# Optimization experiments

Hardware: AMD Instinct MI355X
Metric: run time of the kernel (lower is better)

Reference implementation:

```python
import jax, jax.numpy as jnp
import numpy as np

N = 256      # max_num_nodes (padded nodes per graph)
H = 8        # attention heads
F = 128      # feature_dim
L = 9        # n_layers
INFLA = 6.0  # MCL inflation
EPS = 1e-6


def _layernorm(x, g, b):
    mu = x.mean(-1, keepdims=True)
    var = ((x - mu) ** 2).mean(-1, keepdims=True)
    return (x - mu) / jnp.sqrt(var + 1e-5) * g + b


def _get_mcl(adj):
    # Markov-cluster style power iteration with inflation every 3rd step (num=6)
    m = adj / (adj.sum(-1, keepdims=True) + EPS)
    r = m
    for i in range(6):
        r = m @ r
        if (i + 1) % 3 == 0:
            r = r ** INFLA
        r = r / (r.sum(-1, keepdims=True) + EPS)
    return r


def _forward(input_x, edge_attr, gcn_lin_w, gcn_root_emb, gcn_edge_w,
             gcn_norm_g, gcn_norm_b, ln_in_g, ln_in_b, ln_ffn_g, ln_ffn_b,
             mcl_w, q_w, k_w, v_w, merge_w, merge_b,
             ffn_w1, ffn_b1, ffn_w2, ffn_b2, final_g, final_b,
             edge_index, n_counts, root):
    BN = input_x.shape[0]
    B = BN // N
    dh = F // H
    row, col = edge_index[0], edge_index[1]

    # --- adjacency / padding masks (built once, as in GC_T.forward) ---
    valid = jnp.arange(N)[None, :] < n_counts[:, None]                    # [B,N]
    eb, es, et = row // N, row % N, col % N
    adj = jnp.zeros((B, N, N), bool).at[eb, es, et].set(True)
    adj = adj | (jnp.eye(N, dtype=bool)[None] & valid[:, :, None])        # self loops on valid nodes
    pad = ~(valid[:, :, None] & valid[:, None, :])
    pad_bias = jnp.where(pad, -1024.0, 0.0)[..., None]                    # [B,N,N,1] (broadcast over H)
    mcl = _get_mcl(adj.astype(input_x.dtype))[..., None]                  # [B,N,N,1]

    # --- GCN degree normalization (degree of row index, +1) ---
    deg = jnp.zeros((BN,), input_x.dtype).at[row].add(1.0) + 1.0
    dis = deg ** -0.5
    enorm = (dis[row] * dis[col])[:, None]                                # [E,1]

    out = input_x.reshape(B, N, F)
    for i in range(L):
        # ---- GCNConv: gather-relu-scatter message passing ----
        res = out
        h = out.reshape(BN, F) @ gcn_lin_w[i].T                           # [BN,F]
        ee = edge_attr @ gcn_edge_w[i].T                                  # [E,F]
        msg = enorm * jax.nn.relu(h[row] + ee)                            # x_j = x[row]
        agg = jax.ops.segment_sum(msg, col, num_segments=BN)              # aggregate at target
        g = agg + jax.nn.relu(h + gcn_root_emb[i][root]) / deg[:, None]
        g = jax.nn.relu(_layernorm(g, gcn_norm_g[i], gcn_norm_b[i]))
        out = g.reshape(B, N, F) + res

        # ---- Encoder: biased multi-head attention + FFN ----
        bias4 = (pad_bias + mcl * mcl_w[i][:, 0]).transpose(0, 3, 1, 2)   # [B,H,N,N]
        x = out
        q = (x @ q_w[i].T).reshape(B, N, H, dh).transpose(0, 2, 1, 3) * (dh ** -0.5)
        k = (x @ k_w[i].T).reshape(B, N, H, dh).transpose(0, 2, 1, 3)
        v = (x @ v_w[i].T).reshape(B, N, H, dh).transpose(0, 2, 1, 3)
        att = jax.nn.softmax(jnp.einsum('bhnd,bhmd->bhnm', q, k) + bias4, axis=-1)
        o = jnp.einsum('bhnm,bhmd->bhnd', att, v).transpose(0, 2, 1, 3).reshape(B, N, F)
        o = o @ merge_w[i].T + merge_b[i]
        x = _layernorm(o + x, ln_in_g[i], ln_in_b[i])
        f = jax.nn.gelu(x @ ffn_w1[i].T + ffn_b1[i], approximate=False)
        f = f @ ffn_w2[i].T + ffn_b2[i]
        out = _layernorm(x + f, ln_ffn_g[i], ln_ffn_b[i])

    return _layernorm(out, final_g, final_b)


def setup_inputs() -> dict:
    key = jax.random.key(0)
    ks = jax.random.split(key, 16)
    B, E = 16, 65536
    s = 0.02 * L ** -0.5
    w = lambda k, shape: jax.random.normal(k, shape, jnp.float32) * s
    return {
        'input_x': jax.random.normal(ks[0], (B * N, F), jnp.float32),
        'edge_attr': jax.random.normal(ks[1], (E, 7), jnp.float32),
        'gcn_lin_w': w(ks[2], (L, F, F)),
        'gcn_root_emb': jax.random.normal(ks[3], (L, 2, F), jnp.float32) * 0.02,
        'gcn_edge_w': w(ks[4], (L, F, 7)),
        'gcn_norm_g': jnp.ones((L, F), jnp.float32),
        'gcn_norm_b': jnp.zeros((L, F), jnp.float32),
        'ln_in_g': jnp.ones((L, F), jnp.float32),
        'ln_in_b': jnp.zeros((L, F), jnp.float32),
        'ln_ffn_g': jnp.ones((L, F), jnp.float32),
        'ln_ffn_b': jnp.zeros((L, F), jnp.float32),
        'mcl_w': w(ks[5], (L, H, 1)),
        'q_w': w(ks[6], (L, F, F)),
        'k_w': w(ks[7], (L, F, F)),
        'v_w': w(ks[8], (L, F, F)),
        'merge_w': w(ks[9], (L, F, F)),
        'merge_b': jnp.zeros((L, F), jnp.float32),
        'ffn_w1': w(ks[10], (L, 2 * F, F)),
        'ffn_b1': jnp.zeros((L, 2 * F), jnp.float32),
        'ffn_w2': w(ks[11], (L, F, 2 * F)),
        'ffn_b2': jnp.zeros((L, F), jnp.float32),
        'final_g': jnp.ones((F,), jnp.float32),
        'final_b': jnp.zeros((F,), jnp.float32),
        'edge_index': jax.random.randint(ks[12], (2, E), 0, B * N),
        'n_counts': jax.random.randint(ks[13], (B,), 1, N + 1),
        'root': jax.random.randint(ks[14], (B * N,), 0, 2),
    }


def reference(input_x, edge_attr, gcn_lin_w, gcn_root_emb, gcn_edge_w,
              gcn_norm_g, gcn_norm_b, ln_in_g, ln_in_b, ln_ffn_g, ln_ffn_b,
              mcl_w, q_w, k_w, v_w, merge_w, merge_b,
              ffn_w1, ffn_b1, ffn_w2, ffn_b2, final_g, final_b,
              edge_index, n_counts, root):
    return _forward(input_x, edge_attr, gcn_lin_w, gcn_root_emb, gcn_edge_w,
                    gcn_norm_g, gcn_norm_b, ln_in_g, ln_in_b, ln_ffn_g, ln_ffn_b,
                    mcl_w, q_w, k_w, v_w, merge_w, merge_b,
                    ffn_w1, ffn_b1, ffn_w2, ffn_b2, final_g, final_b,
                    edge_index, n_counts, root)
```

## Files before the change

### kernel.cpp

```cpp
#include <hip/hip_runtime.h>
#include <hip/hip_bf16.h>
#include <math.h>

#define NLAYER 9

typedef unsigned short u16;
typedef __attribute__((ext_vector_type(8))) short short8;
typedef __attribute__((ext_vector_type(4))) float f32x4;

__device__ inline u16 f2bf(float x) {
  unsigned int u = __float_as_uint(x);
  unsigned int r = (u + 0x7fffu + ((u >> 16) & 1u)) >> 16;
  return (u16)r;
}
__device__ inline float gelu_exact(float x) {
  return 0.5f * x * (1.0f + erff(x * 0.7071067811865476f));
}

__global__ void build_adj_kernel(const int* __restrict__ ei, float* __restrict__ adj,
                                 float* __restrict__ deg, int* __restrict__ ccount, int E) {
  int e = blockIdx.x * 256 + threadIdx.x;
  if (e >= E) return;
  int r = ei[e], c = ei[E + e];
  int b = r >> 8;
  adj[((size_t)b << 16) + ((size_t)(r & 255) << 8) + (c & 255)] = 1.0f;
  atomicAdd(&deg[r], 1.0f);
  atomicAdd(&ccount[c], 1);
}

__global__ void selfloop_deg_kernel(const int* __restrict__ nc, float* __restrict__ adj,
                                    float* __restrict__ deg, float* __restrict__ dis) {
  int n = blockIdx.x * 256 + threadIdx.x;
  int b = n >> 8, i = n & 255;
  if (i < nc[b]) adj[((size_t)b << 16) + ((size_t)i << 8) + i] = 1.0f;
  float d = deg[n] + 1.0f;
  deg[n] = d;
  dis[n] = rsqrtf(d);
}

__global__ __launch_bounds__(1024) void scan_kernel(const int* __restrict__ ccount,
                                                    int* __restrict__ rowptr, int n) {
  __shared__ int part[1024];
  int t = threadIdx.x;
  int base = t * 4;
  int c[4], s = 0;
#pragma unroll
  for (int i = 0; i < 4; i++) { c[i] = (base + i < n) ? ccount[base + i] : 0; s += c[i]; }
  part[t] = s;
  __syncthreads();
  for (int o = 1; o < 1024; o <<= 1) {
    int v = (t >= o) ? part[t - o] : 0;
    __syncthreads();
    part[t] += v;
    __syncthreads();
  }
  int excl = part[t] - s;
#pragma unroll
  for (int i = 0; i < 4; i++) {
    if (base + i < n) rowptr[base + i] = excl;
    excl += c[i];
  }
  if (t == 1023) rowptr[n] = part[1023];
}

__global__ void scatter_kernel(const int* __restrict__ ei, const float* __restrict__ dis,
                               const int* __restrict__ rowptr, int* __restrict__ fill,
                               int* __restrict__ src_s, int* __restrict__ eidx_s,
                               float* __restrict__ enorm_s, int E) {
  int e = blockIdx.x * 256 + threadIdx.x;
  if (e >= E) return;
  int r = ei[e], c = ei[E + e];
  int pos = rowptr[c] + atomicAdd(&fill[c], 1);
  src_s[pos] = r;
  eidx_s[pos] = e;
  enorm_s[pos] = dis[r] * dis[c];
}

__global__ __launch_bounds__(256) void norm_rows_kernel(const float* __restrict__ src,
                                                        float* __restrict__ dst) {
  int row = blockIdx.x;
  int t = threadIdx.x;
  float v = src[(size_t)row * 256 + t];
  float s = v;
#pragma unroll
  for (int o = 32; o > 0; o >>= 1) s += __shfl_xor(s, o, 64);
  __shared__ float ws4[4];
  if ((t & 63) == 0) ws4[t >> 6] = s;
  __syncthreads();
  float tot = ws4[0] + ws4[1] + ws4[2] + ws4[3];
  dst[(size_t)row * 256 + t] = v / (tot + 1e-6f);
}

__global__ __launch_bounds__(256) void mcl_prep_kernel(const float* __restrict__ m,
                                                       u16* __restrict__ mb,
                                                       u16* __restrict__ rT) {
  int b = blockIdx.z;
  const float* M = m + ((size_t)b << 16);
  u16* MB = mb + ((size_t)b << 16);
  u16* RT = rT + ((size_t)b << 16);
  int r0 = blockIdx.x * 64, c0 = blockIdx.y * 64;
  __shared__ float ts[64][65];
  int t = threadIdx.x;
  int i = t >> 2, jb = (t & 3) * 16;
#pragma unroll
  for (int g = 0; g < 4; g++) {
    int j = jb + g * 4;
    float4 v = *(const float4*)(M + (size_t)(r0 + i) * 256 + c0 + j);
    ts[i][j] = v.x; ts[i][j + 1] = v.y; ts[i][j + 2] = v.z; ts[i][j + 3] = v.w;
    u16 p4[4] = {f2bf(v.x), f2bf(v.y), f2bf(v.z), f2bf(v.w)};
    *(ushort4*)(MB + (size_t)(r0 + i) * 256 + c0 + j) = *(ushort4*)p4;
  }
  __syncthreads();
#pragma unroll
  for (int g = 0; g < 4; g++) {
    int j = jb + g * 4;
    u16 p4[4] = {f2bf(ts[j][i]), f2bf(ts[j + 1][i]), f2bf(ts[j + 2][i]), f2bf(ts[j + 3][i])};
    *(ushort4*)(RT + (size_t)(c0 + i) * 256 + r0 + j) = *(ushort4*)p4;
  }
}

__global__ __launch_bounds__(256) void mcl_iter_kernel(const u16* __restrict__ rT,
                                                       const u16* __restrict__ mb,
                                                       u16* __restrict__ rTn,
                                                       float* __restrict__ mclr,
                                                       int inflate, int fin) {
  __shared__ float red[64];
  int b = blockIdx.x >> 4, i0 = (blockIdx.x & 15) * 16;
  int w = threadIdx.x >> 6, lane = threadIdx.x & 63;
  int m16 = lane & 15, quad = lane >> 4;
  const u16* A = rT + ((size_t)b << 16);
  const u16* Bm = mb + ((size_t)b << 16);
  f32x4 acc[4];
#pragma unroll
  for (int tj = 0; tj < 4; tj++) acc[tj] = (f32x4){0.f, 0.f, 0.f, 0.f};
  for (int k0 = 0; k0 < 256; k0 += 32) {
    short8 bb = *(const short8*)(Bm + (size_t)(i0 + m16) * 256 + k0 + quad * 8);
#pragma unroll
    for (int tj = 0; tj < 4; tj++) {
      short8 a = *(const short8*)(A + (size_t)(w * 64 + tj * 16 + m16) * 256 + k0 + quad * 8);
      acc[tj] = __builtin_amdgcn_mfma_f32_16x16x32_bf16(a, bb, acc[tj], 0, 0, 0);
    }
  }
  float ps = 0.f;
#pragma unroll
  for (int tj = 0; tj < 4; tj++)
#pragma unroll
    for (int reg = 0; reg < 4; reg++) {
      float v = acc[tj][reg];
      if (inflate) { float v2 = v * v; v = v2 * v2 * v2; }
      acc[tj][reg] = v;
      ps += v;
    }
  ps += __shfl_xor(ps, 16, 64);
  ps += __shfl_xor(ps, 32, 64);
  if (quad == 0) red[w * 16 + m16] = ps;
  __syncthreads();
  float tot = red[m16] + red[16 + m16] + red[32 + m16] + red[48 + m16];
  float inv = 1.f / (tot + 1e-6f);
  if (fin) {
    float* dst = mclr + ((size_t)b << 16);
#pragma unroll
    for (int tj = 0; tj < 4; tj++)
#pragma unroll
      for (int reg = 0; reg < 4; reg++) {
        int j = w * 64 + tj * 16 + quad * 4 + reg;
        dst[(size_t)(i0 + m16) * 256 + j] = acc[tj][reg] * inv;
      }
  } else {
    u16* dst = rTn + ((size_t)b << 16);
#pragma unroll
    for (int tj = 0; tj < 4; tj++)
#pragma unroll
      for (int reg = 0; reg < 4; reg++) {
        int j = w * 64 + tj * 16 + quad * 4 + reg;
        dst[(size_t)j * 256 + i0 + m16] = f2bf(acc[tj][reg] * inv);
      }
  }
}

__global__ void conv_w_kernel(const float* __restrict__ s0, const float* __restrict__ s1,
                              const float* __restrict__ s2, const float* __restrict__ s3,
                              const float* __restrict__ s4, const float* __restrict__ s5,
                              const float* __restrict__ s6, u16* __restrict__ d0,
                              u16* __restrict__ d1, u16* __restrict__ d2,
                              u16* __restrict__ d3, u16* __restrict__ d4,
                              u16* __restrict__ d5, u16* __restrict__ d6) {
  int f = blockIdx.y;
  const float* s;
  u16* d;
  int n;
  switch (f) {
    case 0: s = s0; d = d0; n = NLAYER * 4096; break;
    case 1: s = s1; d = d1; n = NLAYER * 4096; break;
    case 2: s = s2; d = d2; n = NLAYER * 4096; break;
    case 3: s = s3; d = d3; n = NLAYER * 4096; break;
    case 4: s = s4; d = d4; n = NLAYER * 4096; break;
    case 5: s = s5; d = d5; n = NLAYER * 8192; break;
    default: s = s6; d = d6; n = NLAYER * 8192; break;
  }
  int stride = gridDim.x * 256;
  for (int i = blockIdx.x * 256 + threadIdx.x; i < n; i += stride) {
    float4 v = ((const float4*)s)[i];
    u16 p4[4] = {f2bf(v.x), f2bf(v.y), f2bf(v.z), f2bf(v.w)};
    ((ushort4*)d)[i] = *(ushort4*)p4;
  }
}

__global__ __launch_bounds__(256) void copyx_lin_kernel(const float* __restrict__ x,
                                                        const u16* __restrict__ wlin0,
                                                        float* __restrict__ outb,
                                                        float* __restrict__ hbuf) {
  __shared__ u16 st[16 * 136];
  int m0 = blockIdx.x * 16;
  int tid = threadIdx.x;
  int w = tid >> 6, lane = tid & 63;
  int m16 = lane & 15, quad = lane >> 4;
  for (int i = tid; i < 2048; i += 256) {
    int row = i >> 7, col = i & 127;
    float v = x[(size_t)(m0 + row) * 128 + col];
    outb[(size_t)(m0 + row) * 128 + col] = v;
    st[row * 136 + col] = f2bf(v);
  }
  __syncthreads();
  int c0 = w * 32;
  f32x4 acc[2] = {{0.f, 0.f, 0.f, 0.f}, {0.f, 0.f, 0.f, 0.f}};
#pragma unroll
  for (int k0 = 0; k0 < 128; k0 += 32) {
    short8 a = *(const short8*)(st + m16 * 136 + k0 + quad * 8);
#pragma unroll
    for (int t = 0; t < 2; t++) {
      short8 bb = *(const short8*)(wlin0 + (size_t)(c0 + t * 16 + m16) * 128 + k0 + quad * 8);
      acc[t] = __builtin_amdgcn_mfma_f32_16x16x32_bf16(a, bb, acc[t], 0, 0, 0);
    }
  }
#pragma unroll
  for (int t = 0; t < 2; t++)
#pragma unroll
    for (int reg = 0; reg < 4; reg++)
      hbuf[(size_t)(m0 + quad * 4 + reg) * 128 + c0 + t * 16 + m16] = acc[t][reg];
}

__global__ __launch_bounds__(256) void gcn_ln_kernel(
    const int* __restrict__ rowptr, const int* __restrict__ src_s,
    const int* __restrict__ eidx_s, const float* __restrict__ enorm_s,
    const float* __restrict__ ea, const float* __restrict__ We, const float* __restrict__ h,
    const float* __restrict__ remb, const int* __restrict__ root,
    const float* __restrict__ deg, const float* __restrict__ gamma,
    const float* __restrict__ beta, float* __restrict__ out, u16* __restrict__ out16) {
  __shared__ float Wt[7 * 128];
  for (int idx = threadIdx.x; idx < 896; idx += 256) {
    int f = idx & 127, k = idx >> 7;
    Wt[k * 128 + f] = We[f * 7 + k];
  }
  __syncthreads();
  int n = blockIdx.x * 4 + (threadIdx.x >> 6);
  int lane = threadIdx.x & 63;
  int f0 = lane, f1 = lane + 64;
  int p0 = rowptr[n], p1 = rowptr[n + 1];
  float a0 = 0.f, a1 = 0.f;
  int r = 0, e = 0;
  float en = 0.f;
  if (p0 < p1) { r = src_s[p0]; e = eidx_s[p0]; en = enorm_s[p0]; }
  for (int p = p0; p < p1; p++) {
    int rn = 0, enx = 0;
    float ennx = 0.f;
    if (p + 1 < p1) { rn = src_s[p + 1]; enx = eidx_s[p + 1]; ennx = enorm_s[p + 1]; }
    const float* eae = ea + (size_t)e * 7;
    float h0 = h[(size_t)r * 128 + f0];
    float h1 = h[(size_t)r * 128 + f1];
    float d0 = 0.f, d1 = 0.f;
#pragma unroll
    for (int k = 0; k < 7; k++) {
      float ev = eae[k];
      d0 += ev * Wt[k * 128 + f0];
      d1 += ev * Wt[k * 128 + f1];
    }
    a0 += en * fmaxf(h0 + d0, 0.f);
    a1 += en * fmaxf(h1 + d1, 0.f);
    r = rn; e = enx; en = ennx;
  }
  float invd = 1.0f / deg[n];
  const float* re = remb + root[n] * 128;
  size_t base = (size_t)n * 128;
  float g0 = a0 + fmaxf(h[base + f0] + re[f0], 0.f) * invd;
  float g1 = a1 + fmaxf(h[base + f1] + re[f1], 0.f) * invd;
  float s = g0 + g1, ss = g0 * g0 + g1 * g1;
#pragma unroll
  for (int o = 32; o > 0; o >>= 1) { s += __shfl_xor(s, o, 64); ss += __shfl_xor(ss, o, 64); }
  float mu = s * 0.0078125f;
  float var = ss * 0.0078125f - mu * mu;
  float rs = rsqrtf(var + 1e-5f);
  float y0 = fmaxf((g0 - mu) * rs * gamma[f0] + beta[f0], 0.f) + out[base + f0];
  float y1 = fmaxf((g1 - mu) * rs * gamma[f1] + beta[f1], 0.f) + out[base + f1];
  out[base + f0] = y0;
  out[base + f1] = y1;
  out16[base + f0] = f2bf(y0);
  out16[base + f1] = f2bf(y1);
}

__global__ __launch_bounds__(256) void mfma_qkv_kernel(const u16* __restrict__ A,
                                                       const u16* __restrict__ qw,
                                                       const u16* __restrict__ kw,
                                                       const u16* __restrict__ vw,
                                                       float* __restrict__ qkv, int BN) {
  int y = blockIdx.y;
  int which = y >> 2;
  const u16* W = (which == 0) ? qw : (which == 1) ? kw : vw;
  float scale = (which == 0) ? 0.25f : 1.0f;
  float* C = qkv + (size_t)which * BN * 128;
  int m0 = blockIdx.x * 64, o0 = (y & 3) * 32;
  int w = threadIdx.x >> 6, lane = threadIdx.x & 63;
  int m16 = lane & 15, quad = lane >> 4;
  const u16* arow = A + (size_t)(m0 + w * 16 + m16) * 128 + quad * 8;
  const u16* brow0 = W + (size_t)(o0 + m16) * 128 + quad * 8;
  const u16* brow1 = W + (size_t)(o0 + 16 + m16) * 128 + quad * 8;
  f32x4 acc0 = {0.f, 0.f, 0.f, 0.f}, acc1 = {0.f, 0.f, 0.f, 0.f};
#pragma unroll
  for (int k0 = 0; k0 < 128; k0 += 32) {
    short8 a = *(const short8*)(arow + k0);
    acc0 = __builtin_amdgcn_mfma_f32_16x16x32_bf16(a, *(const short8*)(brow0 + k0), acc0, 0, 0, 0);
    acc1 = __builtin_amdgcn_mfma_f32_16x16x32_bf16(a, *(const short8*)(brow1 + k0), acc1, 0, 0, 0);
  }
#pragma unroll
  for (int reg = 0; reg < 4; reg++) {
    int row = m0 + w * 16 + quad * 4 + reg;
    C[(size_t)row * 128 + o0 + m16] = acc0[reg] * scale;
    C[(size_t)row * 128 + o0 + 16 + m16] = acc1[reg] * scale;
  }
}

__global__ __launch_bounds__(256) void attn4_kernel(const float* __restrict__ q,
                                                    const float* __restrict__ k,
                                                    const float* __restrict__ v,
                                                    const float* __restrict__ mclr,
                                                    const float* __restrict__ mclw,
                                                    const int* __restrict__ ncnt,
                                                    u16* __restrict__ o) {
  int qt = blockIdx.x, hh = blockIdx.y, b = blockIdx.z;
  int t = threadIdx.x;
  __shared__ float ks[256][16];
  __shared__ float vs[256][16];
  {
    const float* kp = k + ((size_t)(b * 256 + t) * 128 + hh * 16);
    const float* vp = v + ((size_t)(b * 256 + t) * 128 + hh * 16);
#pragma unroll
    for (int d4 = 0; d4 < 16; d4 += 4) {
      *(float4*)&ks[t][d4] = *(const float4*)(kp + d4);
      *(float4*)&vs[t][d4] = *(const float4*)(vp + d4);
    }
  }
  __syncthreads();
  int i = qt * 64 + (t >> 2);
  int d0 = (t & 3) * 4;
  int nc = ncnt[b];
  bool vi = i < nc;
  float wh = mclw[hh];
  const float* qp = q + ((size_t)(b * 256 + i) * 128 + hh * 16 + d0);
  float qv[4] = {qp[0], qp[1], qp[2], qp[3]};
  const float* mrow = mclr + ((size_t)(b * 256 + i)) * 256;
  float acc[4] = {0.f, 0.f, 0.f, 0.f};
  float lsum = 0.f;
  for (int j0 = 0; j0 < 256; j0 += 4) {
    float4 mc = *(const float4*)(mrow + j0);
    float mcv[4] = {mc.x, mc.y, mc.z, mc.w};
#pragma unroll
    for (int jj = 0; jj < 4; jj++) {
      int j = j0 + jj;
      float s = qv[0] * ks[j][d0] + qv[1] * ks[j][d0 + 1] + qv[2] * ks[j][d0 + 2] +
                qv[3] * ks[j][d0 + 3];
      s += __shfl_xor(s, 1, 64);
      s += __shfl_xor(s, 2, 64);
      float bias = mcv[jj] * wh + ((vi && j >= nc) ? -1024.f : 0.f);
      float pe = __expf(s + bias);
      lsum += pe;
      acc[0] += pe * vs[j][d0];
      acc[1] += pe * vs[j][d0 + 1];
      acc[2] += pe * vs[j][d0 + 2];
      acc[3] += pe * vs[j][d0 + 3];
    }
  }
  float inv = 1.f / lsum;
  u16 p4[4] = {f2bf(acc[0] * inv), f2bf(acc[1] * inv), f2bf(acc[2] * inv), f2bf(acc[3] * inv)};
  *(ushort4*)(o + ((size_t)(b * 256 + i) * 128 + hh * 16 + d0)) = *(ushort4*)p4;
}

__global__ __launch_bounds__(256) void merge_ffn1_kernel(
    const u16* __restrict__ ob16, const u16* __restrict__ Wm, const float* __restrict__ mb,
    const float* __restrict__ outb, const float* __restrict__ gam,
    const float* __restrict__ bet, float* __restrict__ xbuf, const u16* __restrict__ W1,
    const float* __restrict__ b1, u16* __restrict__ f116) {
  __shared__ float redS[64], redSS[64];
  __shared__ u16 st[16 * 136];
  int tid = threadIdx.x;
  int w = tid >> 6, lane = tid & 63;
  int m16 = lane & 15, quad = lane >> 4;
  int m0 = blockIdx.x * 16;
  const u16* arow = ob16 + (size_t)(m0 + m16) * 128 + quad * 8;
  f32x4 acc[2] = {{0.f, 0.f, 0.f, 0.f}, {0.f, 0.f, 0.f, 0.f}};
#pragma unroll
  for (int k0 = 0; k0 < 128; k0 += 32) {
    short8 a = *(const short8*)(arow + k0);
#pragma unroll
    for (int t = 0; t < 2; t++) {
      short8 bb = *(const short8*)(Wm + (size_t)(w * 32 + t * 16 + m16) * 128 + k0 + quad * 8);
      acc[t] = __builtin_amdgcn_mfma_f32_16x16x32_bf16(a, bb, acc[t], 0, 0, 0);
    }
  }
  float s4[4] = {0.f, 0.f, 0.f, 0.f}, ss4[4] = {0.f, 0.f, 0.f, 0.f};
#pragma unroll
  for (int t = 0; t < 2; t++) {
    int col = w * 32 + t * 16 + m16;
    float bi = mb[col];
#pragma unroll
    for (int reg = 0; reg < 4; reg++) {
      int row = m0 + quad * 4 + reg;
      float v = acc[t][reg] + bi + outb[(size_t)row * 128 + col];
      acc[t][reg] = v;
      s4[reg] += v;
      ss4[reg] += v * v;
    }
  }
#pragma unroll
  for (int o = 1; o <= 8; o <<= 1)
#pragma unroll
    for (int reg = 0; reg < 4; reg++) {
      s4[reg] += __shfl_xor(s4[reg], o, 64);
      ss4[reg] += __shfl_xor(ss4[reg], o, 64);
    }
  if (m16 == 0) {
#pragma unroll
    for (int reg = 0; reg < 4; reg++) {
      redS[w * 16 + quad * 4 + reg] = s4[reg];
      redSS[w * 16 + quad * 4 + reg] = ss4[reg];
    }
  }
  __syncthreads();
  float mu[4], rsd[4];
#pragma unroll
  for (int reg = 0; reg < 4; reg++) {
    int r = quad * 4 + reg;
    float S = redS[r] + redS[16 + r] + redS[32 + r] + redS[48 + r];
    float SS = redSS[r] + redSS[16 + r] + redSS[32 + r] + redSS[48 + r];
    mu[reg] = S * 0.0078125f;
    float var = SS * 0.0078125f - mu[reg] * mu[reg];
    rsd[reg] = rsqrtf(var + 1e-5f);
  }
#pragma unroll
  for (int t = 0; t < 2; t++) {
    int col = w * 32 + t * 16 + m16;
    float g = gam[col], be = bet[col];
#pragma unroll
    for (int reg = 0; reg < 4; reg++) {
      int row = m0 + quad * 4 + reg;
      float y = (acc[t][reg] - mu[reg]) * rsd[reg] * g + be;
      xbuf[(size_t)row * 128 + col] = y;
      st[(quad * 4 + reg) * 136 + col] = f2bf(y);
    }
  }
  __syncthreads();
  f32x4 acc1[4];
#pragma unroll
  for (int t = 0; t < 4; t++) acc1[t] = (f32x4){0.f, 0.f, 0.f, 0.f};
#pragma unroll
  for (int k0 = 0; k0 < 128; k0 += 32) {
    short8 a = *(const short8*)(st + m16 * 136 + k0 + quad * 8);
#pragma unroll
    for (int t = 0; t < 4; t++) {
      short8 bb = *(const short8*)(W1 + (size_t)(w * 64 + t * 16 + m16) * 128 + k0 + quad * 8);
      acc1[t] = __builtin_amdgcn_mfma_f32_16x16x32_bf16(a, bb, acc1[t], 0, 0, 0);
    }
  }
#pragma unroll
  for (int t = 0; t < 4; t++) {
    int col = w * 64 + t * 16 + m16;
    float bi = b1[col];
#pragma unroll
    for (int reg = 0; reg < 4; reg++) {
      int row = m0 + quad * 4 + reg;
      f116[(size_t)row * 256 + col] = f2bf(gelu_exact(acc1[t][reg] + bi));
    }
  }
}

__global__ __launch_bounds__(256) void ffn2_lin_kernel(
    const u16* __restrict__ f116, const u16* __restrict__ W2, const float* __restrict__ b2,
    const float* __restrict__ xbuf, const float* __restrict__ gam,
    const float* __restrict__ bet, float* __restrict__ outb, const u16* __restrict__ wlin_next,
    float* __restrict__ hbuf) {
  __shared__ float redS[64], redSS[64];
  __shared__ u16 st[16 * 136];
  int tid = threadIdx.x;
  int w = tid >> 6, lane = tid & 63;
  int m16 = lane & 15, quad = lane >> 4;
  int m0 = blockIdx.x * 16;
  const u16* arow = f116 + (size_t)(m0 + m16) * 256 + quad * 8;
  f32x4 acc[2] = {{0.f, 0.f, 0.f, 0.f}, {0.f, 0.f, 0.f, 0.f}};
#pragma unroll
  for (int k0 = 0; k0 < 256; k0 += 32) {
    short8 a = *(const short8*)(arow + k0);
#pragma unroll
    for (int t = 0; t < 2; t++) {
      short8 bb = *(const short8*)(W2 + (size_t)(w * 32 + t * 16 + m16) * 256 + k0 + quad * 8);
      acc[t] = __builtin_amdgcn_mfma_f32_16x16x32_bf16(a, bb, acc[t], 0, 0, 0);
    }
  }
  float s4[4] = {0.f, 0.f, 0.f, 0.f}, ss4[4] = {0.f, 0.f, 0.f, 0.f};
#pragma unroll
  for (int t = 0; t < 2; t++) {
    int col = w * 32 + t * 16 + m16;
    float bi = b2[col];
#pragma unroll
    for (int reg = 0; reg < 4; reg++) {
      int row = m0 + quad * 4 + reg;
      float v = acc[t][reg] + bi + xbuf[(size_t)row * 128 + col];
      acc[t][reg] = v;
      s4[reg] += v;
      ss4[reg] += v * v;
    }
  }
#pragma unroll
  for (int o = 1; o <= 8; o <<= 1)
#pragma unroll
    for (int reg = 0; reg < 4; reg++) {
      s4[reg] += __shfl_xor(s4[reg], o, 64);
      ss4[reg] += __shfl_xor(ss4[reg], o, 64);
    }
  if (m16 == 0) {
#pragma unroll
    for (int reg = 0; reg < 4; reg++) {
      redS[w * 16 + quad * 4 + reg] = s4[reg];
      redSS[w * 16 + quad * 4 + reg] = ss4[reg];
    }
  }
  __syncthreads();
  float mu[4], rsd[4];
#pragma unroll
  for (int reg = 0; reg < 4; reg++) {
    int r = quad * 4 + reg;
    float S = redS[r] + redS[16 + r] + redS[32 + r] + redS[48 + r];
    float SS = redSS[r] + redSS[16 + r] + redSS[32 + r] + redSS[48 + r];
    mu[reg] = S * 0.0078125f;
    float var = SS * 0.0078125f - mu[reg] * mu[reg];
    rsd[reg] = rsqrtf(var + 1e-5f);
  }
#pragma unroll
  for (int t = 0; t < 2; t++) {
    int col = w * 32 + t * 16 + m16;
    float g = gam[col], be = bet[col];
#pragma unroll
    for (int reg = 0; reg < 4; reg++) {
      int row = m0 + quad * 4 + reg;
      float y = (acc[t][reg] - mu[reg]) * rsd[reg] * g + be;
      outb[(size_t)row * 128 + col] = y;
      st[(quad * 4 + reg) * 136 + col] = f2bf(y);
    }
  }
  __syncthreads();
  if (wlin_next) {
    f32x4 acc2[2] = {{0.f, 0.f, 0.f, 0.f}, {0.f, 0.f, 0.f, 0.f}};
#pragma unroll
    for (int k0 = 0; k0 < 128; k0 += 32) {
      short8 a = *(const short8*)(st + m16 * 136 + k0 + quad * 8);
#pragma unroll
      for (int t = 0; t < 2; t++) {
        short8 bb =
            *(const short8*)(wlin_next + (size_t)(w * 32 + t * 16 + m16) * 128 + k0 + quad * 8);
        acc2[t] = __builtin_amdgcn_mfma_f32_16x16x32_bf16(a, bb, acc2[t], 0, 0, 0);
      }
    }
#pragma unroll
    for (int t = 0; t < 2; t++)
#pragma unroll
      for (int reg = 0; reg < 4; reg++)
        hbuf[(size_t)(m0 + quad * 4 + reg) * 128 + w * 32 + t * 16 + m16] = acc2[t][reg];
  }
}

__global__ __launch_bounds__(256) void ln_kernel(const float* __restrict__ a,
                                                 const float* __restrict__ gamma,
                                                 const float* __restrict__ beta,
                                                 float* __restrict__ dst) {
  int n = blockIdx.x * 4 + (threadIdx.x >> 6);
  int lane = threadIdx.x & 63;
  size_t base = (size_t)n * 128;
  int f0 = lane, f1 = lane + 64;
  float x0 = a[base + f0], x1 = a[base + f1];
  float s = x0 + x1, ss = x0 * x0 + x1 * x1;
#pragma unroll
  for (int o = 32; o > 0; o >>= 1) {
    s += __shfl_xor(s, o, 64);
    ss += __shfl_xor(ss, o, 64);
  }
  float mu = s * 0.0078125f;
  float var = ss * 0.0078125f - mu * mu;
  float rs = rsqrtf(var + 1e-5f);
  dst[base + f0] = (x0 - mu) * rs * gamma[f0] + beta[f0];
  dst[base + f1] = (x1 - mu) * rs * gamma[f1] + beta[f1];
}

extern "C" void kernel_launch(void* const* d_in, const int* in_sizes, int n_in,
                              void* d_out, int out_size, void* d_ws, size_t ws_size,
                              hipStream_t stream) {
  const float* input_x = (const float*)d_in[0];
  const float* edge_attr = (const float*)d_in[1];
  const float* gcn_lin_w = (const float*)d_in[2];
  const float* gcn_root = (const float*)d_in[3];
  const float* gcn_edge_w = (const float*)d_in[4];
  const float* gcn_ng = (const float*)d_in[5];
  const float* gcn_nb = (const float*)d_in[6];
  const float* ln_in_g = (const float*)d_in[7];
  const float* ln_in_b = (const float*)d_in[8];
  const float* ln_ffn_g = (const float*)d_in[9];
  const float* ln_ffn_b = (const float*)d_in[10];
  const float* mcl_w = (const float*)d_in[11];
  const float* q_w = (const float*)d_in[12];
  const float* k_w = (const float*)d_in[13];
  const float* v_w = (const float*)d_in[14];
  const float* merge_w = (const float*)d_in[15];
  const float* merge_b = (const float*)d_in[16];
  const float* ffn_w1 = (const float*)d_in[17];
  const float* ffn_b1 = (const float*)d_in[18];
  const float* ffn_w2 = (const float*)d_in[19];
  const float* ffn_b2 = (const float*)d_in[20];
  const float* final_g = (const float*)d_in[21];
  const float* final_b = (const float*)d_in[22];
  const int* edge_index = (const int*)d_in[23];
  const int* n_counts = (const int*)d_in[24];
  const int* root = (const int*)d_in[25];

  const int E = in_sizes[23] / 2;
  const int B = in_sizes[24];
  const int BN = B * 256;

  float* ws = (float*)d_ws;
  size_t off = 0;
  auto alloc = [&](size_t n) {
    off = (off + 3) & ~(size_t)3;
    float* q = ws + off;
    off += n;
    return q;
  };
  const size_t NN2 = (size_t)B * 256 * 256;
  const size_t XF = (size_t)BN * 128;
  float* mclr = alloc(NN2);
  float* mbuf = alloc(NN2);
  float* rt = alloc(NN2);
  (void)rt;
  float* qkv = mbuf;
  float* hbuf = alloc(XF);
  float* xbuf = alloc(XF);
  float* deg = alloc(BN);
  int* ccount = (int*)alloc(BN);
  int* fill = (int*)alloc(BN);
  float* dis = alloc(BN);
  int* rowptr = (int*)alloc(BN + 1);
  int* src_s = (int*)alloc(E);
  int* eidx_s = (int*)alloc(E);
  float* enorm_s = alloc(E);
  u16* mb16 = (u16*)alloc(NN2 / 2);
  u16* rT16 = (u16*)alloc(NN2 / 2);
  u16* cT16 = (u16*)alloc(NN2 / 2);
  u16* outb16 = (u16*)alloc(XF / 2);
  u16* ob16 = (u16*)alloc(XF / 2);
  u16* f116 = (u16*)alloc(XF);
  u16* wlin16 = (u16*)alloc((size_t)NLAYER * 8192);
  u16* wq16 = (u16*)alloc((size_t)NLAYER * 8192);
  u16* wk16 = (u16*)alloc((size_t)NLAYER * 8192);
  u16* wv16 = (u16*)alloc((size_t)NLAYER * 8192);
  u16* wm16 = (u16*)alloc((size_t)NLAYER * 8192);
  u16* wf116 = (u16*)alloc((size_t)NLAYER * 16384);
  u16* wf216 = (u16*)alloc((size_t)NLAYER * 16384);
  float* outb = (float*)d_out;

  hipMemsetAsync(mbuf, 0, NN2 * sizeof(float), stream);
  hipMemsetAsync(deg, 0, 3 * BN * sizeof(float), stream);
  build_adj_kernel<<<(E + 255) / 256, 256, 0, stream>>>(edge_index, mbuf, deg, ccount, E);
  selfloop_deg_kernel<<<BN / 256, 256, 0, stream>>>(n_counts, mbuf, deg, dis);
  scan_kernel<<<1, 1024, 0, stream>>>(ccount, rowptr, BN);
  scatter_kernel<<<(E + 255) / 256, 256, 0, stream>>>(edge_index, dis, rowptr, fill, src_s,
                                                      eidx_s, enorm_s, E);
  dim3 cwg(72, 7);
  conv_w_kernel<<<cwg, 256, 0, stream>>>(gcn_lin_w, q_w, k_w, v_w, merge_w, ffn_w1, ffn_w2,
                                         wlin16, wq16, wk16, wv16, wm16, wf116, wf216);
  norm_rows_kernel<<<BN, 256, 0, stream>>>(mbuf, mbuf);
  dim3 mmg(4, 4, B);
  mcl_prep_kernel<<<mmg, 256, 0, stream>>>(mbuf, mb16, rT16);
  {
    u16 *cur = rT16, *nxt = cT16;
    for (int it = 0; it < 6; it++) {
      int inflate = (it == 2 || it == 5) ? 1 : 0;
      mcl_iter_kernel<<<16 * B, 256, 0, stream>>>(cur, mb16, nxt, mclr, inflate,
                                                  it == 5 ? 1 : 0);
      u16* tmp = cur;
      cur = nxt;
      nxt = tmp;
    }
  }
  copyx_lin_kernel<<<BN / 16, 256, 0, stream>>>(input_x, wlin16, outb, hbuf);

  dim3 g12(BN / 64, 12);
  dim3 ag(4, 8, B);
  for (int l = 0; l < NLAYER; l++) {
    gcn_ln_kernel<<<BN / 4, 256, 0, stream>>>(
        rowptr, src_s, eidx_s, enorm_s, edge_attr, gcn_edge_w + (size_t)l * 896, hbuf,
        gcn_root + (size_t)l * 256, root, deg, gcn_ng + l * 128, gcn_nb + l * 128, outb,
        outb16);
    mfma_qkv_kernel<<<g12, 256, 0, stream>>>(outb16, wq16 + (size_t)l * 16384,
                                             wk16 + (size_t)l * 16384,
                                             wv16 + (size_t)l * 16384, qkv, BN);
    attn4_kernel<<<ag, 256, 0, stream>>>(qkv, qkv + XF, qkv + 2 * XF, mclr, mcl_w + l * 8,
                                         n_counts, ob16);
    merge_ffn1_kernel<<<BN / 16, 256, 0, stream>>>(
        ob16, wm16 + (size_t)l * 16384, merge_b + l * 128, outb, ln_in_g + l * 128,
        ln_in_b + l * 128, xbuf, wf116 + (size_t)l * 32768, ffn_b1 + l * 256, f116);
    const u16* wnext = (l + 1 < NLAYER) ? (wlin16 + (size_t)(l + 1) * 16384) : nullptr;
    ffn2_lin_kernel<<<BN / 16, 256, 0, stream>>>(
        f116, wf216 + (size_t)l * 32768, ffn_b2 + l * 128, xbuf, ln_ffn_g + l * 128,
        ln_ffn_b + l * 128, outb, wnext, hbuf);
  }
  ln_kernel<<<BN / 4, 256, 0, stream>>>(outb, final_g, final_b, outb);
}
```

Measured before the change: 892.5 us.

## Fuse QKV projection into attention and merge setup kernels and final layernorm

Computes the K/V projection for the whole graph and Q for the tile inside the attention kernel using MFMA. This removes the separate QKV kernel and its fp32 round trip through global memory. Each attention block recomputes K and V for its head, so that projection work is repeated once per query tile. The setup kernels are merged into three combined launches. The final layernorm is folded into the last FFN2 kernel, removing several launches.

```diff
diff --git a/kernel.cpp b/kernel.cpp
--- a/kernel.cpp
+++ b/kernel.cpp
@@ -17,78 +17,118 @@
   return 0.5f * x * (1.0f + erff(x * 0.7071067811865476f));
 }
 
-__global__ void build_adj_kernel(const int* __restrict__ ei, float* __restrict__ adj,
-                                 float* __restrict__ deg, int* __restrict__ ccount, int E) {
-  int e = blockIdx.x * 256 + threadIdx.x;
-  if (e >= E) return;
-  int r = ei[e], c = ei[E + e];
-  int b = r >> 8;
-  adj[((size_t)b << 16) + ((size_t)(r & 255) << 8) + (c & 255)] = 1.0f;
-  atomicAdd(&deg[r], 1.0f);
-  atomicAdd(&ccount[c], 1);
-}
-
-__global__ void selfloop_deg_kernel(const int* __restrict__ nc, float* __restrict__ adj,
-                                    float* __restrict__ deg, float* __restrict__ dis) {
-  int n = blockIdx.x * 256 + threadIdx.x;
-  int b = n >> 8, i = n & 255;
-  if (i < nc[b]) adj[((size_t)b << 16) + ((size_t)i << 8) + i] = 1.0f;
-  float d = deg[n] + 1.0f;
-  deg[n] = d;
-  dis[n] = rsqrtf(d);
-}
-
-__global__ __launch_bounds__(1024) void scan_kernel(const int* __restrict__ ccount,
-                                                    int* __restrict__ rowptr, int n) {
-  __shared__ int part[1024];
+__global__ void setup1_kernel(const int* __restrict__ ei, float* __restrict__ adj,
+                              float* __restrict__ deg, int* __restrict__ ccount, int E, int EB,
+                              const float* __restrict__ s0, const float* __restrict__ s1,
+                              const float* __restrict__ s2, const float* __restrict__ s3,
+                              const float* __restrict__ s4, const float* __restrict__ s5,
+                              const float* __restrict__ s6, u16* __restrict__ d0,
+                              u16* __restrict__ d1, u16* __restrict__ d2,
+                              u16* __restrict__ d3, u16* __restrict__ d4,
+                              u16* __restrict__ d5, u16* __restrict__ d6) {
+  int bid = blockIdx.x;
+  if (bid < EB) {
+    int e = bid * 256 + threadIdx.x;
+    if (e >= E) return;
+    int r = ei[e], c = ei[E + e];
+    int b = r >> 8;
+    adj[((size_t)b << 16) + ((size_t)(r & 255) << 8) + (c & 255)] = 1.0f;
+    atomicAdd(&deg[r], 1.0f);
+    atomicAdd(&ccount[c], 1);
+  } else {
+    int idx = bid - EB;
+    int f = idx / 72, cb = idx % 72;
+    const float* s;
+    u16* d;
+    int n;
+    switch (f) {
+      case 0: s = s0; d = d0; n = NLAYER * 4096; break;
+      case 1: s = s1; d = d1; n = NLAYER * 4096; break;
+      case 2: s = s2; d = d2; n = NLAYER * 4096; break;
+      case 3: s = s3; d = d3; n = NLAYER * 4096; break;
+      case 4: s = s4; d = d4; n = NLAYER * 4096; break;
+      case 5: s = s5; d = d5; n = NLAYER * 8192; break;
+      default: s = s6; d = d6; n = NLAYER * 8192; break;
+    }
+    for (int i = cb * 256 + threadIdx.x; i < n; i += 72 * 256) {
+      float4 v = ((const float4*)s)[i];
+      u16 p4[4] = {f2bf(v.x), f2bf(v.y), f2bf(v.z), f2bf(v.w)};
+      ((ushort4*)d)[i] = *(ushort4*)p4;
+    }
+  }
+}
+
+__global__ __launch_bounds__(1024) void setup2_kernel(const int* __restrict__ nc,
+                                                      float* __restrict__ adj,
+                                                      float* __restrict__ deg,
+                                                      float* __restrict__ dis,
+                                                      const int* __restrict__ ccount,
+                                                      int* __restrict__ rowptr, int BN) {
+  int bid = blockIdx.x;
   int t = threadIdx.x;
-  int base = t * 4;
-  int c[4], s = 0;
-#pragma unroll
-  for (int i = 0; i < 4; i++) { c[i] = (base + i < n) ? ccount[base + i] : 0; s += c[i]; }
-  part[t] = s;
-  __syncthreads();
-  for (int o = 1; o < 1024; o <<= 1) {
-    int v = (t >= o) ? part[t - o] : 0;
+  if (bid < (BN >> 10)) {
+    int n = bid * 1024 + t;
+    int b = n >> 8, i = n & 255;
+    if (i < nc[b]) adj[((size_t)b << 16) + ((size_t)i << 8) + i] = 1.0f;
+    float d = deg[n] + 1.0f;
+    deg[n] = d;
+    dis[n] = rsqrtf(d);
+  } else {
+    __shared__ int part[1024];
+    int base = t * 4;
+    int c[4], s = 0;
+#pragma unroll
+    for (int i = 0; i < 4; i++) { c[i] = (base + i < BN) ? ccount[base + i] : 0; s += c[i]; }
+    part[t] = s;
     __syncthreads();
-    part[t] += v;
-    __syncthreads();
-  }
-  int excl = part[t] - s;
-#pragma unroll
-  for (int i = 0; i < 4; i++) {
-    if (base + i < n) rowptr[base + i] = excl;
-    excl += c[i];
-  }
-  if (t == 1023) rowptr[n] = part[1023];
-}
-
-__global__ void scatter_kernel(const int* __restrict__ ei, const float* __restrict__ dis,
-                               const int* __restrict__ rowptr, int* __restrict__ fill,
-                               int* __restrict__ src_s, int* __restrict__ eidx_s,
-                               float* __restrict__ enorm_s, int E) {
-  int e = blockIdx.x * 256 + threadIdx.x;
-  if (e >= E) return;
-  int r = ei[e], c = ei[E + e];
-  int pos = rowptr[c] + atomicAdd(&fill[c], 1);
-  src_s[pos] = r;
-  eidx_s[pos] = e;
-  enorm_s[pos] = dis[r] * dis[c];
-}
-
-__global__ __launch_bounds__(256) void norm_rows_kernel(const float* __restrict__ src,
-                                                        float* __restrict__ dst) {
-  int row = blockIdx.x;
-  int t = threadIdx.x;
-  float v = src[(size_t)row * 256 + t];
-  float s = v;
-#pragma unroll
-  for (int o = 32; o > 0; o >>= 1) s += __shfl_xor(s, o, 64);
-  __shared__ float ws4[4];
-  if ((t & 63) == 0) ws4[t >> 6] = s;
-  __syncthreads();
-  float tot = ws4[0] + ws4[1] + ws4[2] + ws4[3];
-  dst[(size_t)row * 256 + t] = v / (tot + 1e-6f);
+    for (int o = 1; o < 1024; o <<= 1) {
+      int v = (t >= o) ? part[t - o] : 0;
+      __syncthreads();
+      part[t] += v;
+      __syncthreads();
+    }
+    int excl = part[t] - s;
+#pragma unroll
+    for (int i = 0; i < 4; i++) {
+      if (base + i < BN) rowptr[base + i] = excl;
+      excl += c[i];
+    }
+    if (t == 1023) rowptr[BN] = part[1023];
+  }
+}
+
+__global__ __launch_bounds__(256) void setup3_kernel(float* __restrict__ m,
+                                                     const int* __restrict__ ei,
+                                                     const float* __restrict__ dis,
+                                                     const int* __restrict__ rowptr,
+                                                     int* __restrict__ fill,
+                                                     int* __restrict__ src_s,
+                                                     int* __restrict__ eidx_s,
+                                                     float* __restrict__ enorm_s, int E,
+                                                     int BN) {
+  int bid = blockIdx.x;
+  int w = threadIdx.x >> 6, lane = threadIdx.x & 63;
+  if (bid < (BN >> 2)) {
+    int row = bid * 4 + w;
+    float4 v4 = *(const float4*)(m + (size_t)row * 256 + lane * 4);
+    float s = v4.x + v4.y + v4.z + v4.w;
+#pragma unroll
+    for (int o = 32; o > 0; o >>= 1) s += __shfl_xor(s, o, 64);
+    float inv = 1.f / (s + 1e-6f);
+    v4.x *= inv;
+    v4.y *= inv;
+    v4.z *= inv;
+    v4.w *= inv;
+    *(float4*)(m + (size_t)row * 256 + lane * 4) = v4;
+  } else {
+    int e = (bid - (BN >> 2)) * 256 + threadIdx.x;
+    if (e >= E) return;
+    int r = ei[e], c = ei[E + e];
+    int pos = rowptr[c] + atomicAdd(&fill[c], 1);
+    src_s[pos] = r;
+    eidx_s[pos] = e;
+    enorm_s[pos] = dis[r] * dis[c];
+  }
 }
 
 __global__ __launch_bounds__(256) void mcl_prep_kernel(const float* __restrict__ m,
@@ -175,34 +215,6 @@
         int j = w * 64 + tj * 16 + quad * 4 + reg;
         dst[(size_t)j * 256 + i0 + m16] = f2bf(acc[tj][reg] * inv);
       }
-  }
-}
-
-__global__ void conv_w_kernel(const float* __restrict__ s0, const float* __restrict__ s1,
-                              const float* __restrict__ s2, const float* __restrict__ s3,
-                              const float* __restrict__ s4, const float* __restrict__ s5,
-                              const float* __restrict__ s6, u16* __restrict__ d0,
-                              u16* __restrict__ d1, u16* __restrict__ d2,
-                              u16* __restrict__ d3, u16* __restrict__ d4,
-                              u16* __restrict__ d5, u16* __restrict__ d6) {
-  int f = blockIdx.y;
-  const float* s;
-  u16* d;
-  int n;
-  switch (f) {
-    case 0: s = s0; d = d0; n = NLAYER * 4096; break;
-    case 1: s = s1; d = d1; n = NLAYER * 4096; break;
-    case 2: s = s2; d = d2; n = NLAYER * 4096; break;
-    case 3: s = s3; d = d3; n = NLAYER * 4096; break;
-    case 4: s = s4; d = d4; n = NLAYER * 4096; break;
-    case 5: s = s5; d = d5; n = NLAYER * 8192; break;
-    default: s = s6; d = d6; n = NLAYER * 8192; break;
-  }
-  int stride = gridDim.x * 256;
-  for (int i = blockIdx.x * 256 + threadIdx.x; i < n; i += stride) {
-    float4 v = ((const float4*)s)[i];
-    u16 p4[4] = {f2bf(v.x), f2bf(v.y), f2bf(v.z), f2bf(v.w)};
-    ((ushort4*)d)[i] = *(ushort4*)p4;
   }
 }
 
@@ -298,56 +310,47 @@
   out16[base + f1] = f2bf(y1);
 }
 
-__global__ __launch_bounds__(256) void mfma_qkv_kernel(const u16* __restrict__ A,
-                                                       const u16* __restrict__ qw,
-                                                       const u16* __restrict__ kw,
-                                                       const u16* __restrict__ vw,
-                                                       float* __restrict__ qkv, int BN) {
-  int y = blockIdx.y;
-  int which = y >> 2;
-  const u16* W = (which == 0) ? qw : (which == 1) ? kw : vw;
-  float scale = (which == 0) ? 0.25f : 1.0f;
-  float* C = qkv + (size_t)which * BN * 128;
-  int m0 = blockIdx.x * 64, o0 = (y & 3) * 32;
-  int w = threadIdx.x >> 6, lane = threadIdx.x & 63;
-  int m16 = lane & 15, quad = lane >> 4;
-  const u16* arow = A + (size_t)(m0 + w * 16 + m16) * 128 + quad * 8;
-  const u16* brow0 = W + (size_t)(o0 + m16) * 128 + quad * 8;
-  const u16* brow1 = W + (size_t)(o0 + 16 + m16) * 128 + quad * 8;
-  f32x4 acc0 = {0.f, 0.f, 0.f, 0.f}, acc1 = {0.f, 0.f, 0.f, 0.f};
-#pragma unroll
-  for (int k0 = 0; k0 < 128; k0 += 32) {
-    short8 a = *(const short8*)(arow + k0);
-    acc0 = __builtin_amdgcn_mfma_f32_16x16x32_bf16(a, *(const short8*)(brow0 + k0), acc0, 0, 0, 0);
-    acc1 = __builtin_amdgcn_mfma_f32_16x16x32_bf16(a, *(const short8*)(brow1 + k0), acc1, 0, 0, 0);
-  }
-#pragma unroll
-  for (int reg = 0; reg < 4; reg++) {
-    int row = m0 + w * 16 + quad * 4 + reg;
-    C[(size_t)row * 128 + o0 + m16] = acc0[reg] * scale;
-    C[(size_t)row * 128 + o0 + 16 + m16] = acc1[reg] * scale;
-  }
-}
-
-__global__ __launch_bounds__(256) void attn4_kernel(const float* __restrict__ q,
-                                                    const float* __restrict__ k,
-                                                    const float* __restrict__ v,
-                                                    const float* __restrict__ mclr,
-                                                    const float* __restrict__ mclw,
-                                                    const int* __restrict__ ncnt,
-                                                    u16* __restrict__ o) {
+__global__ __launch_bounds__(256) void attn_qkv_kernel(
+    const u16* __restrict__ x16, const u16* __restrict__ wq, const u16* __restrict__ wk,
+    const u16* __restrict__ wv, const float* __restrict__ mclr,
+    const float* __restrict__ mclw, const int* __restrict__ ncnt, u16* __restrict__ o) {
+  __shared__ float ks[256][16];
+  __shared__ float vs[256][16];
+  __shared__ float qs[64][16];
   int qt = blockIdx.x, hh = blockIdx.y, b = blockIdx.z;
   int t = threadIdx.x;
-  __shared__ float ks[256][16];
-  __shared__ float vs[256][16];
+  int w = t >> 6, lane = t & 63;
+  int m16 = lane & 15, quad = lane >> 4;
+  const u16* bk = wk + (size_t)(hh * 16 + m16) * 128 + quad * 8;
+  const u16* bv = wv + (size_t)(hh * 16 + m16) * 128 + quad * 8;
+#pragma unroll
+  for (int tj = 0; tj < 4; tj++) {
+    int rb = w * 64 + tj * 16;
+    const u16* arow = x16 + (size_t)(b * 256 + rb + m16) * 128 + quad * 8;
+    f32x4 ak = {0.f, 0.f, 0.f, 0.f}, av = {0.f, 0.f, 0.f, 0.f};
+#pragma unroll
+    for (int k0 = 0; k0 < 128; k0 += 32) {
+      short8 a = *(const short8*)(arow + k0);
+      ak = __builtin_amdgcn_mfma_f32_16x16x32_bf16(a, *(const short8*)(bk + k0), ak, 0, 0, 0);
+      av = __builtin_amdgcn_mfma_f32_16x16x32_bf16(a, *(const short8*)(bv + k0), av, 0, 0, 0);
+    }
+#pragma unroll
+    for (int reg = 0; reg < 4; reg++) {
+      ks[rb + quad * 4 + reg][m16] = ak[reg];
+      vs[rb + quad * 4 + reg][m16] = av[reg];
+    }
+  }
   {
-    const float* kp = k + ((size_t)(b * 256 + t) * 128 + hh * 16);
-    const float* vp = v + ((size_t)(b * 256 + t) * 128 + hh * 16);
-#pragma unroll
-    for (int d4 = 0; d4 < 16; d4 += 4) {
-      *(float4*)&ks[t][d4] = *(const float4*)(kp + d4);
-      *(float4*)&vs[t][d4] = *(const float4*)(vp + d4);
-    }
+    const u16* bq = wq + (size_t)(hh * 16 + m16) * 128 + quad * 8;
+    const u16* arow = x16 + (size_t)(b * 256 + qt * 64 + w * 16 + m16) * 128 + quad * 8;
+    f32x4 aq = {0.f, 0.f, 0.f, 0.f};
+#pragma unroll
+    for (int k0 = 0; k0 < 128; k0 += 32) {
+      short8 a = *(const short8*)(arow + k0);
+      aq = __builtin_amdgcn_mfma_f32_16x16x32_bf16(a, *(const short8*)(bq + k0), aq, 0, 0, 0);
+    }
+#pragma unroll
+    for (int reg = 0; reg < 4; reg++) qs[w * 16 + quad * 4 + reg][m16] = aq[reg] * 0.25f;
   }
   __syncthreads();
   int i = qt * 64 + (t >> 2);
@@ -355,8 +358,7 @@
   int nc = ncnt[b];
   bool vi = i < nc;
   float wh = mclw[hh];
-  const float* qp = q + ((size_t)(b * 256 + i) * 128 + hh * 16 + d0);
-  float qv[4] = {qp[0], qp[1], qp[2], qp[3]};
+  float qv[4] = {qs[t >> 2][d0], qs[t >> 2][d0 + 1], qs[t >> 2][d0 + 2], qs[t >> 2][d0 + 3]};
   const float* mrow = mclr + ((size_t)(b * 256 + i)) * 256;
   float acc[4] = {0.f, 0.f, 0.f, 0.f};
   float lsum = 0.f;
@@ -486,7 +488,7 @@
     const u16* __restrict__ f116, const u16* __restrict__ W2, const float* __restrict__ b2,
     const float* __restrict__ xbuf, const float* __restrict__ gam,
     const float* __restrict__ bet, float* __restrict__ outb, const u16* __restrict__ wlin_next,
-    float* __restrict__ hbuf) {
+    float* __restrict__ hbuf, const float* __restrict__ fing, const float* __restrict__ finb) {
   __shared__ float redS[64], redSS[64];
   __shared__ u16 st[16 * 136];
   int tid = threadIdx.x;
@@ -548,9 +550,63 @@
     int col = w * 32 + t * 16 + m16;
     float g = gam[col], be = bet[col];
 #pragma unroll
+    for (int reg = 0; reg < 4; reg++)
+      acc[t][reg] = (acc[t][reg] - mu[reg]) * rsd[reg] * g + be;
+  }
+  if (fing) {
+    float s2[4] = {0.f, 0.f, 0.f, 0.f}, ss2[4] = {0.f, 0.f, 0.f, 0.f};
+#pragma unroll
+    for (int t = 0; t < 2; t++)
+#pragma unroll
+      for (int reg = 0; reg < 4; reg++) {
+        float v = acc[t][reg];
+        s2[reg] += v;
+        ss2[reg] += v * v;
+      }
+#pragma unroll
+    for (int o = 1; o <= 8; o <<= 1)
+#pragma unroll
+      for (int reg = 0; reg < 4; reg++) {
+        s2[reg] += __shfl_xor(s2[reg], o, 64);
+        ss2[reg] += __shfl_xor(ss2[reg], o, 64);
+      }
+    __syncthreads();
+    if (m16 == 0) {
+#pragma unroll
+      for (int reg = 0; reg < 4; reg++) {
+        redS[w * 16 + quad * 4 + reg] = s2[reg];
+        redSS[w * 16 + quad * 4 + reg] = ss2[reg];
+      }
+    }
+    __syncthreads();
+#pragma unroll
+    for (int reg = 0; reg < 4; reg++) {
+      int r = quad * 4 + reg;
+      float S = redS[r] + redS[16 + r] + redS[32 + r] + redS[48 + r];
+      float SS = redSS[r] + redSS[16 + r] + redSS[32 + r] + redSS[48 + r];
+      mu[reg] = S * 0.0078125f;
+      float var = SS * 0.0078125f - mu[reg] * mu[reg];
+      rsd[reg] = rsqrtf(var + 1e-5f);
+    }
+#pragma unroll
+    for (int t = 0; t < 2; t++) {
+      int col = w * 32 + t * 16 + m16;
+      float g = fing[col], be = finb[col];
+#pragma unroll
+      for (int reg = 0; reg < 4; reg++) {
+        int row = m0 + quad * 4 + reg;
+        outb[(size_t)row * 128 + col] = (acc[t][reg] - mu[reg]) * rsd[reg] * g + be;
+      }
+    }
+    return;
+  }
+#pragma unroll
+  for (int t = 0; t < 2; t++) {
+    int col = w * 32 + t * 16 + m16;
+#pragma unroll
     for (int reg = 0; reg < 4; reg++) {
       int row = m0 + quad * 4 + reg;
-      float y = (acc[t][reg] - mu[reg]) * rsd[reg] * g + be;
+      float y = acc[t][reg];
       outb[(size_t)row * 128 + col] = y;
       st[(quad * 4 + reg) * 136 + col] = f2bf(y);
     }
@@ -574,28 +630,6 @@
       for (int reg = 0; reg < 4; reg++)
         hbuf[(size_t)(m0 + quad * 4 + reg) * 128 + w * 32 + t * 16 + m16] = acc2[t][reg];
   }
-}
-
-__global__ __launch_bounds__(256) void ln_kernel(const float* __restrict__ a,
-                                                 const float* __restrict__ gamma,
-                                                 const float* __restrict__ beta,
-                                                 float* __restrict__ dst) {
-  int n = blockIdx.x * 4 + (threadIdx.x >> 6);
-  int lane = threadIdx.x & 63;
-  size_t base = (size_t)n * 128;
-  int f0 = lane, f1 = lane + 64;
-  float x0 = a[base + f0], x1 = a[base + f1];
-  float s = x0 + x1, ss = x0 * x0 + x1 * x1;
-#pragma unroll
-  for (int o = 32; o > 0; o >>= 1) {
-    s += __shfl_xor(s, o, 64);
-    ss += __shfl_xor(ss, o, 64);
-  }
-  float mu = s * 0.0078125f;
-  float var = ss * 0.0078125f - mu * mu;
-  float rs = rsqrtf(var + 1e-5f);
-  dst[base + f0] = (x0 - mu) * rs * gamma[f0] + beta[f0];
-  dst[base + f1] = (x1 - mu) * rs * gamma[f1] + beta[f1];
 }
 
 extern "C" void kernel_launch(void* const* d_in, const int* in_sizes, int n_in,
@@ -631,6 +665,7 @@
   const int E = in_sizes[23] / 2;
   const int B = in_sizes[24];
   const int BN = B * 256;
+  const int EB = (E + 255) / 256;
 
   float* ws = (float*)d_ws;
   size_t off = 0;
@@ -644,9 +679,6 @@
   const size_t XF = (size_t)BN * 128;
   float* mclr = alloc(NN2);
   float* mbuf = alloc(NN2);
-  float* rt = alloc(NN2);
-  (void)rt;
-  float* qkv = mbuf;
   float* hbuf = alloc(XF);
   float* xbuf = alloc(XF);
   float* deg = alloc(BN);
@@ -660,8 +692,8 @@
   u16* mb16 = (u16*)alloc(NN2 / 2);
   u16* rT16 = (u16*)alloc(NN2 / 2);
   u16* cT16 = (u16*)alloc(NN2 / 2);
+  u16* ob16 = (u16*)alloc(XF / 2);
   u16* outb16 = (u16*)alloc(XF / 2);
-  u16* ob16 = (u16*)alloc(XF / 2);
   u16* f116 = (u16*)alloc(XF);
   u16* wlin16 = (u16*)alloc((size_t)NLAYER * 8192);
   u16* wq16 = (u16*)alloc((size_t)NLAYER * 8192);
@@ -674,15 +706,13 @@
 
   hipMemsetAsync(mbuf, 0, NN2 * sizeof(float), stream);
   hipMemsetAsync(deg, 0, 3 * BN * sizeof(float), stream);
-  build_adj_kernel<<<(E + 255) / 256, 256, 0, stream>>>(edge_index, mbuf, deg, ccount, E);
-  selfloop_deg_kernel<<<BN / 256, 256, 0, stream>>>(n_counts, mbuf, deg, dis);
-  scan_kernel<<<1, 1024, 0, stream>>>(ccount, rowptr, BN);
-  scatter_kernel<<<(E + 255) / 256, 256, 0, stream>>>(edge_index, dis, rowptr, fill, src_s,
-                                                      eidx_s, enorm_s, E);
-  dim3 cwg(72, 7);
-  conv_w_kernel<<<cwg, 256, 0, stream>>>(gcn_lin_w, q_w, k_w, v_w, merge_w, ffn_w1, ffn_w2,
-                                         wlin16, wq16, wk16, wv16, wm16, wf116, wf216);
-  norm_rows_kernel<<<BN, 256, 0, stream>>>(mbuf, mbuf);
+  setup1_kernel<<<EB + 504, 256, 0, stream>>>(edge_index, mbuf, deg, ccount, E, EB, gcn_lin_w,
+                                              q_w, k_w, v_w, merge_w, ffn_w1, ffn_w2, wlin16,
+                                              wq16, wk16, wv16, wm16, wf116, wf216);
+  setup2_kernel<<<BN / 1024 + 1, 1024, 0, stream>>>(n_counts, mbuf, deg, dis, ccount, rowptr,
+                                                    BN);
+  setup3_kernel<<<BN / 4 + EB, 256, 0, stream>>>(mbuf, edge_index, dis, rowptr, fill, src_s,
+                                                 eidx_s, enorm_s, E, BN);
   dim3 mmg(4, 4, B);
   mcl_prep_kernel<<<mmg, 256, 0, stream>>>(mbuf, mb16, rT16);
   {
@@ -698,25 +728,24 @@
   }
   copyx_lin_kernel<<<BN / 16, 256, 0, stream>>>(input_x, wlin16, outb, hbuf);
 
-  dim3 g12(BN / 64, 12);
   dim3 ag(4, 8, B);
   for (int l = 0; l < NLAYER; l++) {
     gcn_ln_kernel<<<BN / 4, 256, 0, stream>>>(
         rowptr, src_s, eidx_s, enorm_s, edge_attr, gcn_edge_w + (size_t)l * 896, hbuf,
         gcn_root + (size_t)l * 256, root, deg, gcn_ng + l * 128, gcn_nb + l * 128, outb,
         outb16);
-    mfma_qkv_kernel<<<g12, 256, 0, stream>>>(outb16, wq16 + (size_t)l * 16384,
-                                             wk16 + (size_t)l * 16384,
-                                             wv16 + (size_t)l * 16384, qkv, BN);
-    attn4_kernel<<<ag, 256, 0, stream>>>(qkv, qkv + XF, qkv + 2 * XF, mclr, mcl_w + l * 8,
-                                         n_counts, ob16);
+    attn_qkv_kernel<<<ag, 256, 0, stream>>>(outb16, wq16 + (size_t)l * 16384,
+                                            wk16 + (size_t)l * 16384,
+                                            wv16 + (size_t)l * 16384, mclr, mcl_w + l * 8,
+                                            n_counts, ob16);
     merge_ffn1_kernel<<<BN / 16, 256, 0, stream>>>(
         ob16, wm16 + (size_t)l * 16384, merge_b + l * 128, outb, ln_in_g + l * 128,
         ln_in_b + l * 128, xbuf, wf116 + (size_t)l * 32768, ffn_b1 + l * 256, f116);
     const u16* wnext = (l + 1 < NLAYER) ? (wlin16 + (size_t)(l + 1) * 16384) : nullptr;
+    const float* fg = (l == NLAYER - 1) ? final_g : nullptr;
+    const float* fb = (l == NLAYER - 1) ? final_b : nullptr;
     ffn2_lin_kernel<<<BN / 16, 256, 0, stream>>>(
         f116, wf216 + (size_t)l * 32768, ffn_b2 + l * 128, xbuf, ln_ffn_g + l * 128,
-        ln_ffn_b + l * 128, outb, wnext, hbuf);
-  }
-  ln_kernel<<<BN / 4, 256, 0, stream>>>(outb, final_g, final_b, outb);
-}
+        ln_ffn_b + l * 128, outb, wnext, hbuf, fg, fb);
+  }
+}
```

Measured after the change: 864.4 us. 1.03x faster.
